# Optimization experiments

Measured on AMD Instinct MI355X. Metric: run time of the kernel, lower is better.

## Reference

```python
import jax, jax.numpy as jnp
import numpy as np

N = 50000      # num_nodes
E = 640000     # num_edges
IN = 128       # in_dim
OUT = 128      # out_dim
H = 4          # num_heads
DH = OUT // H  # head_dim = 32
R = 5          # num_relations


def setup_inputs() -> dict:
    key = jax.random.key(0)
    k0, k1, k2, k3 = jax.random.split(key, 4)
    x = jax.random.normal(k0, (N, IN), dtype=jnp.float32)
    # stacked per-relation Linear weights/biases (Linear(in_dim, H*DH))
    Ws = jax.random.normal(k1, (R, IN, H * DH), dtype=jnp.float32) * (1.0 / np.sqrt(IN))
    bs = jnp.zeros((R, H * DH), dtype=jnp.float32)
    edge_index = jax.random.randint(k2, (2, E), 0, N)
    edge_types = jax.random.randint(k3, (E,), 0, R)
    return {"x": x, "Ws": Ws, "bs": bs, "edge_index": edge_index, "edge_types": edge_types}


def reference(x, Ws, bs, edge_index, edge_types):
    """Per-relation linear -> gather(src) -> scatter-add(dst) -> mean, then concat.

    Faithful to GraphAttentionLayer.forward with concat=True (att params are
    unused in the original forward; dropout is identity at inference).
    """
    src, dst = edge_index[0], edge_index[1]
    outs = []
    for r in range(R):  # small fixed relation count
        mask = (edge_types == r)
        mf = mask.astype(x.dtype)  # [E]
        x_r = (x @ Ws[r] + bs[r]).reshape(N, H, DH)          # [N,H,DH]
        msgs = x_r[src] * mf[:, None, None]                   # [E,H,DH] masked gather
        agg = jax.ops.segment_sum(msgs, dst, num_segments=N)  # scatter-add
        deg = jnp.clip(jax.ops.segment_sum(mf, dst, num_segments=N), 1.0)  # bincount.clamp(1)
        outs.append(agg / deg[:, None, None])
    out = jnp.concatenate(outs, axis=-1)  # [N, H, DH*R], DH*R=160 != OUT
    out = out.reshape(N, -1)[:, :OUT]     # view + truncate path of original
    return out
```

## Files before the change

### kernel.cpp

```cpp
#include <hip/hip_runtime.h>

#define GN 50000
#define GE 640000
#define CAPR 16
#define NPLACE 625
#define NGEMM 1563
#define NGRP 313

typedef __attribute__((ext_vector_type(8))) short short8;
typedef __attribute__((ext_vector_type(4))) float float4v;

static __device__ __forceinline__ unsigned short f2bf(float f) {
    union { float f; unsigned u; } v; v.f = f;
    unsigned r = v.u + 0x7FFF + ((v.u >> 16) & 1);
    return (unsigned short)(r >> 16);
}
static __device__ __forceinline__ float bf2f(unsigned short h) {
    union { unsigned u; float f; } v; v.u = ((unsigned)h) << 16;
    return v.f;
}

__global__ __launch_bounds__(256) void prep_kernel(const float* __restrict__ Ws,
                                                   unsigned short* __restrict__ Wtg,
                                                   int* __restrict__ cnt) {
    int i = blockIdx.x * 256 + threadIdx.x;
    if (i < GN * 4) cnt[i] = 0;
    if (i < 128 * 128) {
        int n = i >> 7, k = i & 127;
        Wtg[n * 128 + k] = f2bf(Ws[(n >> 5) * 16384 + k * 128 + (n & 31)]);
    }
}

__global__ __launch_bounds__(256) void combo_kernel(const float* __restrict__ x,
                                                    const unsigned short* __restrict__ Wtg,
                                                    const float* __restrict__ bs,
                                                    unsigned short* __restrict__ yb,
                                                    const int* __restrict__ ei,
                                                    const int* __restrict__ et,
                                                    int* __restrict__ cnt,
                                                    unsigned short* __restrict__ elist) {
    const int b = blockIdx.x;
    const int t = threadIdx.x;
    const int grp = b / 7;
    const int role = b % 7;

    if (role < 2) {
        int p = grp * 2 + role;
        if (p >= NPLACE) return;
        int e = p * 1024 + t * 4;
        int4 r4 = *(const int4*)(et + e);
        int4 s4 = *(const int4*)(ei + e);
        int4 d4 = *(const int4*)(ei + GE + e);
        if (r4.x < 4) {
            int pos = atomicAdd(&cnt[(d4.x << 2) + r4.x], 1);
            if (pos < CAPR) elist[(d4.x << 6) + (r4.x << 4) + pos] = (unsigned short)s4.x;
        }
        if (r4.y < 4) {
            int pos = atomicAdd(&cnt[(d4.y << 2) + r4.y], 1);
            if (pos < CAPR) elist[(d4.y << 6) + (r4.y << 4) + pos] = (unsigned short)s4.y;
        }
        if (r4.z < 4) {
            int pos = atomicAdd(&cnt[(d4.z << 2) + r4.z], 1);
            if (pos < CAPR) elist[(d4.z << 6) + (r4.z << 4) + pos] = (unsigned short)s4.z;
        }
        if (r4.w < 4) {
            int pos = atomicAdd(&cnt[(d4.w << 2) + r4.w], 1);
            if (pos < CAPR) elist[(d4.w << 6) + (r4.w << 4) + pos] = (unsigned short)s4.w;
        }
        return;
    }

    const int tile = grp * 5 + (role - 2);
    if (tile >= NGEMM) return;
    const int wv   = t >> 6;
    const int lane = t & 63;
    const int m    = lane & 15;
    const int quad = lane >> 4;
    const int row0 = tile * 32 + (wv & 1) * 16;
    const int col0 = (wv >> 1) * 64;

    short8 afr[4];
    {
        int grow = row0 + m;
        if (grow > GN - 1) grow = GN - 1;
        const float* xr = x + (size_t)grow * 128 + quad * 8;
        #pragma unroll
        for (int s = 0; s < 4; s++) {
            float4 u0 = *(const float4*)(xr + s * 32);
            float4 u1 = *(const float4*)(xr + s * 32 + 4);
            short8 a;
            a[0] = (short)f2bf(u0.x); a[1] = (short)f2bf(u0.y);
            a[2] = (short)f2bf(u0.z); a[3] = (short)f2bf(u0.w);
            a[4] = (short)f2bf(u1.x); a[5] = (short)f2bf(u1.y);
            a[6] = (short)f2bf(u1.z); a[7] = (short)f2bf(u1.w);
            afr[s] = a;
        }
    }

    float4v acc[4] = {{0.f,0.f,0.f,0.f},{0.f,0.f,0.f,0.f},
                      {0.f,0.f,0.f,0.f},{0.f,0.f,0.f,0.f}};
    #pragma unroll
    for (int c = 0; c < 4; c++) {
        const unsigned short* wb = Wtg + (size_t)(col0 + c * 16 + m) * 128 + quad * 8;
        short8 b0 = *(const short8*)(wb);
        short8 b1 = *(const short8*)(wb + 32);
        short8 b2 = *(const short8*)(wb + 64);
        short8 b3 = *(const short8*)(wb + 96);
        acc[c] = __builtin_amdgcn_mfma_f32_16x16x32_bf16(afr[0], b0, acc[c], 0, 0, 0);
        acc[c] = __builtin_amdgcn_mfma_f32_16x16x32_bf16(afr[1], b1, acc[c], 0, 0, 0);
        acc[c] = __builtin_amdgcn_mfma_f32_16x16x32_bf16(afr[2], b2, acc[c], 0, 0, 0);
        acc[c] = __builtin_amdgcn_mfma_f32_16x16x32_bf16(afr[3], b3, acc[c], 0, 0, 0);
    }

    #pragma unroll
    for (int c = 0; c < 4; c++) {
        int n = col0 + c * 16 + m;
        float bias = bs[(n >> 5) * 128 + (n & 31)];
        #pragma unroll
        for (int reg = 0; reg < 4; reg++) {
            int grow = row0 + quad * 4 + reg;
            if (grow < GN)
                yb[(size_t)grow * 128 + n] = f2bf(acc[c][reg] + bias);
        }
    }
}

__global__ __launch_bounds__(256) void accum_kernel(const unsigned short* __restrict__ yb,
                                                    const int* __restrict__ cnt,
                                                    const unsigned short* __restrict__ elist,
                                                    float* __restrict__ out) {
    int node = blockIdx.x * 8 + (threadIdx.x >> 5);
    int lane = threadIdx.x & 31;
    if (node >= GN) return;
    int4 c4 = *(const int4*)(cnt + (node << 2));
    int pw = ((const int*)(elist + (node << 6)))[lane];

    int d0 = c4.x < CAPR ? c4.x : CAPR;
    int d1 = c4.y < CAPR ? c4.y : CAPR;
    int d2 = c4.z < CAPR ? c4.z : CAPR;
    int d3 = c4.w < CAPR ? c4.w : CAPR;
    int m01 = d0 > d1 ? d0 : d1;
    int m23 = d2 > d3 ? d2 : d3;
    int dmax = m01 > m23 ? m01 : m23;

    const unsigned short* y0 = yb + lane;
    float a0 = 0.f, a1 = 0.f, a2 = 0.f, a3 = 0.f;

    #pragma unroll 4
    for (int j = 0; j < CAPR; ++j) {
        if (j >= dmax) break;
        int w0 = __shfl(pw,      (j >> 1), 32);
        int w1 = __shfl(pw,  8 + (j >> 1), 32);
        int w2 = __shfl(pw, 16 + (j >> 1), 32);
        int w3 = __shfl(pw, 24 + (j >> 1), 32);
        int sh = (j & 1) << 4;
        int s0 = (w0 >> sh) & 0xFFFF;
        int s1 = (w1 >> sh) & 0xFFFF;
        int s2 = (w2 >> sh) & 0xFFFF;
        int s3 = (w3 >> sh) & 0xFFFF;
        float v0 = bf2f(y0[(s0 << 7)     ]);
        float v1 = bf2f(y0[(s1 << 7) + 32]);
        float v2 = bf2f(y0[(s2 << 7) + 64]);
        float v3 = bf2f(y0[(s3 << 7) + 96]);
        a0 += (j < d0) ? v0 : 0.f;
        a1 += (j < d1) ? v1 : 0.f;
        a2 += (j < d2) ? v2 : 0.f;
        a3 += (j < d3) ? v3 : 0.f;
    }

    float* o = out + (size_t)node * 128;
    o[      lane] = a0 / (float)(c4.x > 1 ? c4.x : 1);
    o[ 32 + lane] = a1 / (float)(c4.y > 1 ? c4.y : 1);
    o[ 64 + lane] = a2 / (float)(c4.z > 1 ? c4.z : 1);
    o[ 96 + lane] = a3 / (float)(c4.w > 1 ? c4.w : 1);
}

extern "C" void kernel_launch(void* const* d_in, const int* in_sizes, int n_in,
                              void* d_out, int out_size, void* d_ws, size_t ws_size,
                              hipStream_t stream) {
    const float* x  = (const float*)d_in[0];
    const float* Ws = (const float*)d_in[1];
    const float* bs = (const float*)d_in[2];
    const int*   ei = (const int*)d_in[3];
    const int*   et = (const int*)d_in[4];

    float* out = (float*)d_out;
    char* ws = (char*)d_ws;
    unsigned short* yb    = (unsigned short*)ws;
    unsigned short* Wtg   = yb + (size_t)GN * 128;
    int* cnt              = (int*)(Wtg + 128 * 128);
    unsigned short* elist = (unsigned short*)(cnt + GN * 4);

    prep_kernel<<<(GN * 4 + 255) / 256, 256, 0, stream>>>(Ws, Wtg, cnt);
    combo_kernel<<<NGRP * 7, 256, 0, stream>>>(x, Wtg, bs, yb, ei, et, cnt, elist);
    accum_kernel<<<(GN + 7) / 8, 256, 0, stream>>>(yb, cnt, elist, out);
}
```

Measured before the change: 135.2 us.

## Replace global per-node atomic edge placement with two-stage bucketed binning

```diff
diff --git a/kernel.cpp b/kernel.cpp
--- a/kernel.cpp
+++ b/kernel.cpp
@@ -3,7 +3,8 @@
 #define GN 50000
 #define GE 640000
 #define CAPR 16
-#define NPLACE 625
+#define NBUCK 196
+#define BCAP 4096
 #define NGEMM 1563
 #define NGRP 313
 
@@ -22,9 +23,9 @@
 
 __global__ __launch_bounds__(256) void prep_kernel(const float* __restrict__ Ws,
                                                    unsigned short* __restrict__ Wtg,
-                                                   int* __restrict__ cnt) {
+                                                   int* __restrict__ bucket_cnt) {
     int i = blockIdx.x * 256 + threadIdx.x;
-    if (i < GN * 4) cnt[i] = 0;
+    if (i < NBUCK) bucket_cnt[i] = 0;
     if (i < 128 * 128) {
         int n = i >> 7, k = i & 127;
         Wtg[n * 128 + k] = f2bf(Ws[(n >> 5) * 16384 + k * 128 + (n & 31)]);
@@ -37,40 +38,61 @@
                                                     unsigned short* __restrict__ yb,
                                                     const int* __restrict__ ei,
                                                     const int* __restrict__ et,
-                                                    int* __restrict__ cnt,
-                                                    unsigned short* __restrict__ elist) {
+                                                    int* __restrict__ bucket_cnt,
+                                                    unsigned* __restrict__ bucket_buf) {
+    __shared__ int hist[NBUCK];
+    __shared__ int base[NBUCK];
     const int b = blockIdx.x;
     const int t = threadIdx.x;
-    const int grp = b / 7;
-    const int role = b % 7;
-
-    if (role < 2) {
-        int p = grp * 2 + role;
-        if (p >= NPLACE) return;
-        int e = p * 1024 + t * 4;
-        int4 r4 = *(const int4*)(et + e);
-        int4 s4 = *(const int4*)(ei + e);
-        int4 d4 = *(const int4*)(ei + GE + e);
-        if (r4.x < 4) {
-            int pos = atomicAdd(&cnt[(d4.x << 2) + r4.x], 1);
-            if (pos < CAPR) elist[(d4.x << 6) + (r4.x << 4) + pos] = (unsigned short)s4.x;
-        }
-        if (r4.y < 4) {
-            int pos = atomicAdd(&cnt[(d4.y << 2) + r4.y], 1);
-            if (pos < CAPR) elist[(d4.y << 6) + (r4.y << 4) + pos] = (unsigned short)s4.y;
-        }
-        if (r4.z < 4) {
-            int pos = atomicAdd(&cnt[(d4.z << 2) + r4.z], 1);
-            if (pos < CAPR) elist[(d4.z << 6) + (r4.z << 4) + pos] = (unsigned short)s4.z;
-        }
-        if (r4.w < 4) {
-            int pos = atomicAdd(&cnt[(d4.w << 2) + r4.w], 1);
-            if (pos < CAPR) elist[(d4.w << 6) + (r4.w << 4) + pos] = (unsigned short)s4.w;
+    const int grp = b / 6;
+    const int role = b % 6;
+
+    if (role == 0) {
+        int e = grp * 2048 + t * 8;
+        bool act = (e < GE);
+        for (int i = t; i < NBUCK; i += 256) hist[i] = 0;
+        __syncthreads();
+
+        int ky[8], rk[8];
+        unsigned rc[8];
+        bool vd[8];
+        if (act) {
+            int4 ra = *(const int4*)(et + e);
+            int4 rb = *(const int4*)(et + e + 4);
+            int4 sa = *(const int4*)(ei + e);
+            int4 sb = *(const int4*)(ei + e + 4);
+            int4 da = *(const int4*)(ei + GE + e);
+            int4 db = *(const int4*)(ei + GE + e + 4);
+            int rr[8] = {ra.x, ra.y, ra.z, ra.w, rb.x, rb.y, rb.z, rb.w};
+            int ss[8] = {sa.x, sa.y, sa.z, sa.w, sb.x, sb.y, sb.z, sb.w};
+            int dd[8] = {da.x, da.y, da.z, da.w, db.x, db.y, db.z, db.w};
+            #pragma unroll
+            for (int j = 0; j < 8; j++) {
+                vd[j] = rr[j] < 4;
+                ky[j] = dd[j] >> 8;
+                rc[j] = (unsigned)ss[j] | ((unsigned)rr[j] << 16)
+                      | ((unsigned)(dd[j] & 255) << 18);
+                rk[j] = vd[j] ? atomicAdd(&hist[ky[j]], 1) : 0;
+            }
+        } else {
+            #pragma unroll
+            for (int j = 0; j < 8; j++) { vd[j] = false; ky[j] = 0; rk[j] = 0; rc[j] = 0; }
+        }
+        __syncthreads();
+        for (int i = t; i < NBUCK; i += 256)
+            base[i] = hist[i] ? atomicAdd(&bucket_cnt[i], hist[i]) : 0;
+        __syncthreads();
+        #pragma unroll
+        for (int j = 0; j < 8; j++) {
+            if (vd[j]) {
+                int pos = base[ky[j]] + rk[j];
+                if (pos < BCAP) bucket_buf[ky[j] * BCAP + pos] = rc[j];
+            }
         }
         return;
     }
 
-    const int tile = grp * 5 + (role - 2);
+    const int tile = grp * 5 + (role - 1);
     if (tile >= NGEMM) return;
     const int wv   = t >> 6;
     const int lane = t & 63;
@@ -123,6 +145,40 @@
                 yb[(size_t)grow * 128 + n] = f2bf(acc[c][reg] + bias);
         }
     }
+}
+
+__global__ __launch_bounds__(256) void stage2_kernel(const int* __restrict__ bucket_cnt,
+                                                     const unsigned* __restrict__ bucket_buf,
+                                                     int* __restrict__ cnt,
+                                                     unsigned short* __restrict__ elist) {
+    __shared__ unsigned short lel[256 * 64];
+    __shared__ int lcn[256 * 4];
+    const int b = blockIdx.x;
+    const int t = threadIdx.x;
+
+    for (int i = t; i < 256 * 4; i += 256) lcn[i] = 0;
+    for (int i = t; i < 256 * 32; i += 256) ((unsigned*)lel)[i] = 0;
+    __syncthreads();
+
+    int nb = bucket_cnt[b];
+    if (nb > BCAP) nb = BCAP;
+    const unsigned* bp = bucket_buf + b * BCAP;
+    for (int i = t; i < nb; i += 256) {
+        unsigned w = bp[i];
+        int s  = w & 0xFFFF;
+        int r  = (w >> 16) & 3;
+        int dl = (w >> 18) & 255;
+        int pos = atomicAdd(&lcn[(dl << 2) + r], 1);
+        if (pos < CAPR) lel[(dl << 6) + (r << 4) + pos] = (unsigned short)s;
+    }
+    __syncthreads();
+
+    int n0 = b << 8;
+    int nn = GN - n0; if (nn > 256) nn = 256;
+    unsigned* eg = (unsigned*)(elist + ((size_t)n0 << 6));
+    for (int i = t; i < nn * 32; i += 256) eg[i] = ((unsigned*)lel)[i];
+    int* cg = cnt + (n0 << 2);
+    for (int i = t; i < nn * 4; i += 256) cg[i] = lcn[i];
 }
 
 __global__ __launch_bounds__(256) void accum_kernel(const unsigned short* __restrict__ yb,
@@ -190,8 +246,12 @@
     unsigned short* Wtg   = yb + (size_t)GN * 128;
     int* cnt              = (int*)(Wtg + 128 * 128);
     unsigned short* elist = (unsigned short*)(cnt + GN * 4);
-
-    prep_kernel<<<(GN * 4 + 255) / 256, 256, 0, stream>>>(Ws, Wtg, cnt);
-    combo_kernel<<<NGRP * 7, 256, 0, stream>>>(x, Wtg, bs, yb, ei, et, cnt, elist);
+    int* bucket_cnt       = (int*)(elist + (size_t)GN * 64);
+    unsigned* bucket_buf  = (unsigned*)(bucket_cnt + 256);
+
+    prep_kernel<<<64, 256, 0, stream>>>(Ws, Wtg, bucket_cnt);
+    combo_kernel<<<NGRP * 6, 256, 0, stream>>>(x, Wtg, bs, yb, ei, et,
+                                               bucket_cnt, bucket_buf);
+    stage2_kernel<<<NBUCK, 256, 0, stream>>>(bucket_cnt, bucket_buf, cnt, elist);
     accum_kernel<<<(GN + 7) / 8, 256, 0, stream>>>(yb, cnt, elist, out);
 }
```

New measurement: 134.5 us. Within noise of the previous version (-0.6%).
